# Optimization experiments

Hardware: AMD Instinct MI355X
Metric: run time of the kernel (lower is better)

## Reference

```python
import jax, jax.numpy as jnp
import numpy as np

NEG_SLOPE = 0.2
MASK_FILL = -9e10


def setup_inputs() -> dict:
    key = jax.random.key(0)
    ks = jax.random.split(key, 9)
    B, n_ope, n_mac = 32, 2048, 1024
    total = 64
    ope_dim, mac_dim, out_dim = 64, 64, 128
    ope_ma_adj = jax.random.randint(ks[0], (total, n_ope, n_mac), 0, 2, dtype=jnp.int32)
    batch_idxes = jax.random.randint(ks[1], (B,), 0, total, dtype=jnp.int64)
    feat_ope = jax.random.normal(ks[2], (B, n_ope, ope_dim), dtype=jnp.float32)
    feat_mac = jax.random.normal(ks[3], (B, n_mac, mac_dim), dtype=jnp.float32)
    # parameters (xavier-normal-like scaling)
    def xavier(k, shape):
        fan_in, fan_out = shape[1], shape[0]
        std = jnp.sqrt(2.0 / (fan_in + fan_out))
        return std * jax.random.normal(k, shape, dtype=jnp.float32)
    ope_w = xavier(ks[4], (out_dim, ope_dim))   # Linear weight [out, in]
    mac_w = xavier(ks[5], (out_dim, mac_dim))
    ope_alpha = xavier(ks[6], (out_dim, 1))
    mac_alpha = xavier(ks[7], (out_dim, 1))
    res_w = xavier(ks[8], (out_dim, mac_dim))
    return {
        "ope_ma_adj": ope_ma_adj, "batch_idxes": batch_idxes,
        "feat_ope": feat_ope, "feat_mac": feat_mac,
        "ope_w": ope_w, "mac_w": mac_w,
        "ope_alpha": ope_alpha, "mac_alpha": mac_alpha, "res_w": res_w,
    }


def reference(ope_ma_adj, batch_idxes, feat_ope, feat_mac,
              ope_w, mac_w, ope_alpha, mac_alpha, res_w):
    # dropout p=0 -> identity
    h_ope = jnp.einsum('bod,kd->bok', feat_ope, ope_w)   # [B, n_ope, out]
    h_mac = jnp.einsum('bmd,kd->bmk', feat_mac, mac_w)   # [B, n_mac, out]
    attn_ope = jnp.einsum('bok,k->bo', h_ope, ope_alpha[:, 0])  # [B, n_ope]
    attn_mac = jnp.einsum('bmk,k->bm', h_mac, mac_alpha[:, 0])  # [B, n_mac]
    e = attn_ope[:, :, None] + attn_mac[:, None, :]             # [B, n_ope, n_mac]
    e = jnp.where(e >= 0, e, NEG_SLOPE * e)                      # leaky relu
    mask = ope_ma_adj[batch_idxes] == 1                          # [B, n_ope, n_mac]
    e = jnp.where(mask, e, MASK_FILL)
    alpha = jax.nn.softmax(e, axis=-2)                           # over operations
    out = jnp.einsum('bom,bok->bmk', alpha, h_ope)               # [B, n_mac, out]
    h_res = jnp.einsum('bmd,kd->bmk', feat_mac, res_w)
    return out + h_res
```

## Files before the change

### kernel.cpp

```cpp
#include <hip/hip_runtime.h>

#define N_OPE 2048
#define N_MAC 1024
#define DIM   64
#define KOUT  128
#define NB    32

typedef __attribute__((ext_vector_type(8))) short short8;
typedef __attribute__((ext_vector_type(4))) float floatx4;

static __device__ __forceinline__ unsigned short f2bf(float f) {
    unsigned int u = __builtin_bit_cast(unsigned int, f);
    u += 0x7fffu + ((u >> 16) & 1u);
    return (unsigned short)(u >> 16);
}
static __device__ __forceinline__ float bf2f(unsigned short h) {
    unsigned int u = ((unsigned int)h) << 16;
    return __builtin_bit_cast(float, u);
}

__global__ __launch_bounds__(256, 2) void k_ope(const float* __restrict__ feat,
        const float* __restrict__ w, const float* __restrict__ alpha,
        unsigned short* __restrict__ h_f, float2* __restrict__ pq)
{
    int wid = threadIdx.x >> 6, lane = threadIdx.x & 63;
    int L = lane & 15, q = lane >> 4;
    int base = blockIdx.x * 128 + wid * 32;
    int b = base >> 11;
    int o0w = base & (N_OPE - 1);

    float fA[2][2][8];
    #pragma unroll
    for (int mf = 0; mf < 2; ++mf) {
        const float* fr = feat + (size_t)(base + mf * 16 + L) * DIM + q * 8;
        #pragma unroll
        for (int ks = 0; ks < 2; ++ks) {
            float4 v0 = *(const float4*)(fr + ks * 32);
            float4 v1 = *(const float4*)(fr + ks * 32 + 4);
            fA[mf][ks][0] = v0.x; fA[mf][ks][1] = v0.y; fA[mf][ks][2] = v0.z; fA[mf][ks][3] = v0.w;
            fA[mf][ks][4] = v1.x; fA[mf][ks][5] = v1.y; fA[mf][ks][6] = v1.z; fA[mf][ks][7] = v1.w;
        }
    }

    short8 Ah[2][2], Al[2][2];
    #pragma unroll
    for (int mf = 0; mf < 2; ++mf)
        #pragma unroll
        for (int ks = 0; ks < 2; ++ks)
            #pragma unroll
            for (int j = 0; j < 8; ++j) {
                float x = fA[mf][ks][j];
                unsigned short h = f2bf(x);
                Ah[mf][ks][j] = (short)h;
                Al[mf][ks][j] = (short)f2bf(x - bf2f(h));
            }

    floatx4 C[2][8];
    #pragma unroll
    for (int mf = 0; mf < 2; ++mf)
        #pragma unroll
        for (int nf = 0; nf < 8; ++nf) C[mf][nf] = (floatx4)0.f;

    #pragma unroll
    for (int ks = 0; ks < 2; ++ks) {
        #pragma unroll
        for (int nf = 0; nf < 8; ++nf) {
            const float* wp = w + (size_t)(nf * 16 + L) * DIM + ks * 32 + q * 8;
            float4 u0 = *(const float4*)(wp);
            float4 u1 = *(const float4*)(wp + 4);
            float bw[8] = {u0.x, u0.y, u0.z, u0.w, u1.x, u1.y, u1.z, u1.w};
            short8 Bh, Bl;
            #pragma unroll
            for (int j = 0; j < 8; ++j) {
                unsigned short h = f2bf(bw[j]);
                Bh[j] = (short)h;
                Bl[j] = (short)f2bf(bw[j] - bf2f(h));
            }
            #pragma unroll
            for (int mf = 0; mf < 2; ++mf) {
                C[mf][nf] = __builtin_amdgcn_mfma_f32_16x16x32_bf16(Ah[mf][ks], Bh, C[mf][nf], 0, 0, 0);
                C[mf][nf] = __builtin_amdgcn_mfma_f32_16x16x32_bf16(Al[mf][ks], Bh, C[mf][nf], 0, 0, 0);
                C[mf][nf] = __builtin_amdgcn_mfma_f32_16x16x32_bf16(Ah[mf][ks], Bl, C[mf][nf], 0, 0, 0);
            }
        }
    }

    float alf[8];
    #pragma unroll
    for (int nf = 0; nf < 8; ++nf) alf[nf] = alpha[nf * 16 + L];
    #pragma unroll
    for (int mf = 0; mf < 2; ++mf) {
        #pragma unroll
        for (int r = 0; r < 4; ++r) {
            float s = 0.f;
            #pragma unroll
            for (int nf = 0; nf < 8; ++nf) s = fmaf(C[mf][nf][r], alf[nf], s);
            s += __shfl_xor(s, 1); s += __shfl_xor(s, 2);
            s += __shfl_xor(s, 4); s += __shfl_xor(s, 8);
            if (L == 0)
                pq[base + mf * 16 + q * 4 + r] = make_float2(__expf(s), __expf(0.2f * s));
        }
    }

    __shared__ unsigned short T[4][128 * 40];
    #pragma unroll
    for (int mf = 0; mf < 2; ++mf)
        #pragma unroll
        for (int nf = 0; nf < 8; ++nf)
            #pragma unroll
            for (int r = 0; r < 4; ++r)
                T[wid][(nf * 16 + L) * 40 + mf * 16 + q * 4 + r] = f2bf(C[mf][nf][r]);
    __syncthreads();

    int oc = o0w >> 5;
    unsigned short* dst = h_f + ((((size_t)b * 64 + oc) * 8) * 64 + lane) * 8;
    #pragma unroll
    for (int nf = 0; nf < 8; ++nf) {
        short8 v = *(const short8*)&T[wid][(nf * 16 + L) * 40 + q * 8];
        *(short8*)(dst + (size_t)nf * 512) = v;
    }
}

__global__ __launch_bounds__(256) void k_attn(const int* __restrict__ adj,
        const int* __restrict__ bidx,
        const unsigned short* __restrict__ h_f,
        const float2* __restrict__ pq,
        const float* __restrict__ feat_mac,
        const float* __restrict__ mac_w, const float* __restrict__ mac_alpha,
        const float* __restrict__ res_w,
        float* __restrict__ out)
{
    int b  = blockIdx.y;
    int m0 = blockIdx.x * 32;
    int t = threadIdx.x, wv = t >> 6, lane = t & 63;
    int L = lane & 15, q = lane >> 4;

    __shared__ float buf0[32 * 132];
    __shared__ float buf1[32 * 132];
    __shared__ float waS[64];
    __shared__ float amS[32];
    __shared__ float DS[4][32];

    {
        int d = t & 63, seg = t >> 6;
        float p = 0.f;
        #pragma unroll 8
        for (int n = seg * 32; n < seg * 32 + 32; ++n)
            p = fmaf(mac_w[n * DIM + d], mac_alpha[n], p);
        buf0[seg * 64 + d] = p;
    }
    __syncthreads();
    if (t < 64) waS[t] = buf0[t] + buf0[64 + t] + buf0[128 + t] + buf0[192 + t];
    __syncthreads();
    {
        int row = t & 31, seg = t >> 5;
        const float* fr = feat_mac + ((size_t)b * N_MAC + m0 + row) * DIM + seg * 8;
        float p = 0.f;
        #pragma unroll
        for (int k = 0; k < 8; ++k) p = fmaf(fr[k], waS[seg * 8 + k], p);
        buf1[seg * 32 + row] = p;
    }
    __syncthreads();
    if (t < 32) {
        float s = 0.f;
        #pragma unroll
        for (int sg = 0; sg < 8; ++sg) s += buf1[sg * 32 + t];
        amS[t] = s;
    }
    __syncthreads();

    float2 amv = *(const float2*)&amS[2 * L];
    float pM0 = __expf(amv.x), qM0 = __expf(0.2f * amv.x);
    float pM1 = __expf(amv.y), qM1 = __expf(0.2f * amv.y);

    const int* adjt = adj + (size_t)bidx[b] * (N_OPE * N_MAC);
    const unsigned short* hfb = h_f + (size_t)b * (64 * 8 * 64 * 8);
    const float2* pqb = pq + (size_t)b * N_OPE;

    floatx4 C0[8], C1[8];
    #pragma unroll
    for (int i = 0; i < 8; ++i) { C0[i] = (floatx4)0.f; C1[i] = (floatx4)0.f; }
    float den0 = 0.f, den1 = 0.f;

    int oBeg = wv * (N_OPE / 4);
    for (int o0 = oBeg; o0 < oBeg + N_OPE / 4; o0 += 32) {
        int ob = o0 + q * 8;
        float4 pv0 = *(const float4*)(pqb + ob);
        float4 pv1 = *(const float4*)(pqb + ob + 2);
        float4 pv2 = *(const float4*)(pqb + ob + 4);
        float4 pv3 = *(const float4*)(pqb + ob + 6);
        float pA[8] = {pv0.x, pv0.z, pv1.x, pv1.z, pv2.x, pv2.z, pv3.x, pv3.z};
        float qA[8] = {pv0.y, pv0.w, pv1.y, pv1.w, pv2.y, pv2.w, pv3.y, pv3.w};

        int2 mk[8];
        #pragma unroll
        for (int j = 0; j < 8; ++j)
            mk[j] = *(const int2*)(adjt + (size_t)(ob + j) * N_MAC + m0 + 2 * L);

        const unsigned short* fp = hfb + (((size_t)(o0 >> 5) * 8) * 64 + lane) * 8;
        short8 Bf[8];
        #pragma unroll
        for (int nf = 0; nf < 8; ++nf)
            Bf[nf] = *(const short8*)(fp + (size_t)nf * 512);

        float w0v[8], w1v[8];
        #pragma unroll
        for (int j = 0; j < 8; ++j) {
            float tp0 = pA[j] * pM0;
            float w0 = (tp0 >= 1.0f) ? tp0 : qA[j] * qM0;
            w0 = (mk[j].x == 1) ? w0 : 0.f;
            den0 += w0; w0v[j] = w0;
            float tp1 = pA[j] * pM1;
            float w1 = (tp1 >= 1.0f) ? tp1 : qA[j] * qM1;
            w1 = (mk[j].y == 1) ? w1 : 0.f;
            den1 += w1; w1v[j] = w1;
        }
        int4 A0i, A1i;
        #pragma unroll
        for (int j2 = 0; j2 < 4; ++j2) {
            unsigned lo0 = __builtin_bit_cast(unsigned, w0v[2 * j2])     + 0x8000u;
            unsigned hi0 = __builtin_bit_cast(unsigned, w0v[2 * j2 + 1]) + 0x8000u;
            ((unsigned*)&A0i)[j2] = __builtin_amdgcn_perm(hi0, lo0, 0x07060302u);
            unsigned lo1 = __builtin_bit_cast(unsigned, w1v[2 * j2])     + 0x8000u;
            unsigned hi1 = __builtin_bit_cast(unsigned, w1v[2 * j2 + 1]) + 0x8000u;
            ((unsigned*)&A1i)[j2] = __builtin_amdgcn_perm(hi1, lo1, 0x07060302u);
        }
        short8 A0 = __builtin_bit_cast(short8, A0i);
        short8 A1 = __builtin_bit_cast(short8, A1i);

        #pragma unroll
        for (int nf = 0; nf < 8; ++nf) {
            C0[nf] = __builtin_amdgcn_mfma_f32_16x16x32_bf16(A0, Bf[nf], C0[nf], 0, 0, 0);
            C1[nf] = __builtin_amdgcn_mfma_f32_16x16x32_bf16(A1, Bf[nf], C1[nf], 0, 0, 0);
        }
    }

    den0 += __shfl_xor(den0, 16); den0 += __shfl_xor(den0, 32);
    den1 += __shfl_xor(den1, 16); den1 += __shfl_xor(den1, 32);
    if (q == 0) { DS[wv][L] = den0; DS[wv][16 + L] = den1; }

    if (wv == 0 || wv == 2) {
        float* bp = (wv == 0) ? buf0 : buf1;
        #pragma unroll
        for (int mf = 0; mf < 2; ++mf) {
            const floatx4* Cf = mf ? C1 : C0;
            #pragma unroll
            for (int nf = 0; nf < 8; ++nf)
                #pragma unroll
                for (int r = 0; r < 4; ++r)
                    bp[(mf * 16 + q * 4 + r) * 132 + nf * 16 + L] = Cf[nf][r];
        }
    }
    __syncthreads();
    if (wv == 1 || wv == 3) {
        float* bp = (wv == 1) ? buf0 : buf1;
        #pragma unroll
        for (int mf = 0; mf < 2; ++mf) {
            const floatx4* Cf = mf ? C1 : C0;
            #pragma unroll
            for (int nf = 0; nf < 8; ++nf)
                #pragma unroll
                for (int r = 0; r < 4; ++r)
                    bp[(mf * 16 + q * 4 + r) * 132 + nf * 16 + L] += Cf[nf][r];
        }
    }
    __syncthreads();

    float fA[2][2][8];
    #pragma unroll
    for (int mf = 0; mf < 2; ++mf) {
        const float* fr = feat_mac + ((size_t)b * N_MAC + m0 + 2 * L + mf) * DIM + q * 8;
        #pragma unroll
        for (int ks = 0; ks < 2; ++ks) {
            float4 v0 = *(const float4*)(fr + ks * 32);
            float4 v1 = *(const float4*)(fr + ks * 32 + 4);
            fA[mf][ks][0] = v0.x; fA[mf][ks][1] = v0.y; fA[mf][ks][2] = v0.z; fA[mf][ks][3] = v0.w;
            fA[mf][ks][4] = v1.x; fA[mf][ks][5] = v1.y; fA[mf][ks][6] = v1.z; fA[mf][ks][7] = v1.w;
        }
    }
    short8 Ah[2][2], Al[2][2];
    #pragma unroll
    for (int mf = 0; mf < 2; ++mf)
        #pragma unroll
        for (int ks = 0; ks < 2; ++ks)
            #pragma unroll
            for (int j = 0; j < 8; ++j) {
                float x = fA[mf][ks][j];
                unsigned short h = f2bf(x);
                Ah[mf][ks][j] = (short)h;
                Al[mf][ks][j] = (short)f2bf(x - bf2f(h));
            }
    floatx4 R[2][2];
    R[0][0] = (floatx4)0.f; R[0][1] = (floatx4)0.f;
    R[1][0] = (floatx4)0.f; R[1][1] = (floatx4)0.f;
    #pragma unroll
    for (int ks = 0; ks < 2; ++ks) {
        #pragma unroll
        for (int nfl = 0; nfl < 2; ++nfl) {
            const float* wp = res_w + (size_t)((wv * 2 + nfl) * 16 + L) * DIM + ks * 32 + q * 8;
            float4 u0 = *(const float4*)(wp);
            float4 u1 = *(const float4*)(wp + 4);
            float bw[8] = {u0.x, u0.y, u0.z, u0.w, u1.x, u1.y, u1.z, u1.w};
            short8 Bh, Bl;
            #pragma unroll
            for (int j = 0; j < 8; ++j) {
                unsigned short h = f2bf(bw[j]);
                Bh[j] = (short)h;
                Bl[j] = (short)f2bf(bw[j] - bf2f(h));
            }
            #pragma unroll
            for (int mf = 0; mf < 2; ++mf) {
                R[mf][nfl] = __builtin_amdgcn_mfma_f32_16x16x32_bf16(Ah[mf][ks], Bh, R[mf][nfl], 0, 0, 0);
                R[mf][nfl] = __builtin_amdgcn_mfma_f32_16x16x32_bf16(Al[mf][ks], Bh, R[mf][nfl], 0, 0, 0);
                R[mf][nfl] = __builtin_amdgcn_mfma_f32_16x16x32_bf16(Ah[mf][ks], Bl, R[mf][nfl], 0, 0, 0);
            }
        }
    }

    #pragma unroll
    for (int mf = 0; mf < 2; ++mf) {
        #pragma unroll
        for (int r = 0; r < 4; ++r) {
            int fragrow = q * 4 + r;
            int m = m0 + 2 * fragrow + mf;
            float inv = 1.0f / (DS[0][mf * 16 + fragrow] + DS[1][mf * 16 + fragrow]
                              + DS[2][mf * 16 + fragrow] + DS[3][mf * 16 + fragrow]);
            size_t obase = ((size_t)b * N_MAC + m) * KOUT;
            #pragma unroll
            for (int nfl = 0; nfl < 2; ++nfl) {
                int col = (wv * 2 + nfl) * 16 + L;
                float num = buf0[(mf * 16 + fragrow) * 132 + col]
                          + buf1[(mf * 16 + fragrow) * 132 + col];
                out[obase + col] = num * inv + R[mf][nfl][r];
            }
        }
    }
}

extern "C" void kernel_launch(void* const* d_in, const int* in_sizes, int n_in,
                              void* d_out, int out_size, void* d_ws, size_t ws_size,
                              hipStream_t stream) {
    const int*   adj       = (const int*)d_in[0];
    const int*   bidx      = (const int*)d_in[1];
    const float* feat_ope  = (const float*)d_in[2];
    const float* feat_mac  = (const float*)d_in[3];
    const float* ope_w     = (const float*)d_in[4];
    const float* mac_w     = (const float*)d_in[5];
    const float* ope_alpha = (const float*)d_in[6];
    const float* mac_alpha = (const float*)d_in[7];
    const float* res_w     = (const float*)d_in[8];
    float* out = (float*)d_out;

    char* ws = (char*)d_ws;
    unsigned short* h_f = (unsigned short*)ws;
    float2* pq          = (float2*)(ws + (size_t)(16 << 20));

    k_ope<<<512, 256, 0, stream>>>(feat_ope, ope_w, ope_alpha, h_f, pq);
    k_attn<<<dim3(N_MAC / 32, NB), 256, 0, stream>>>(adj, bidx, h_f, pq, feat_mac,
                                                     mac_w, mac_alpha, res_w, out);
}
```

Measured before the change: 692.0 us.

## Bit-pack adjacency mask in prep kernel and read packed bits in attention

Adds extra blocks to the projection kernel that read each gathered int32 adjacency row once and pack it into 64-bit bitmasks in workspace. The attention kernel then reads one 64-bit word per operation row instead of int2 pairs from the full int32 adjacency. Before, each of the 32 mac-column blocks per batch read its own strided slice of the int32 rows. The change is meant to replace those scattered narrow loads with a single coalesced full-row pass, at the cost of a packed-mask write and read in between and a larger prep launch.

```diff
diff --git a/kernel.cpp b/kernel.cpp
--- a/kernel.cpp
+++ b/kernel.cpp
@@ -19,11 +19,47 @@
     return __builtin_bit_cast(float, u);
 }
 
-__global__ __launch_bounds__(256, 2) void k_ope(const float* __restrict__ feat,
+__global__ __launch_bounds__(256, 2) void k_prep(const float* __restrict__ feat,
         const float* __restrict__ w, const float* __restrict__ alpha,
-        unsigned short* __restrict__ h_f, float2* __restrict__ pq)
+        unsigned short* __restrict__ h_f, float2* __restrict__ pq,
+        const int* __restrict__ adj, const int* __restrict__ bidx,
+        unsigned long long* __restrict__ pk)
 {
     int wid = threadIdx.x >> 6, lane = threadIdx.x & 63;
+
+    if (blockIdx.x >= 512) {
+        int wave = (blockIdx.x - 512) * 4 + wid;
+        int r0 = wave * 32;
+        int b = r0 >> 11;
+        int o0 = r0 & (N_OPE - 1);
+        const int* at = adj + (size_t)bidx[b] * ((size_t)N_OPE * N_MAC);
+        unsigned long long* dst = pk + ((size_t)b * N_OPE + o0) * 16;
+        int L4 = (lane & 15) * 4;
+        #pragma unroll 2
+        for (int i = 0; i < 32; ++i) {
+            const int* rp = at + (size_t)(o0 + i) * N_MAC + lane * 16;
+            int4 a0 = *(const int4*)(rp);
+            int4 a1 = *(const int4*)(rp + 4);
+            int4 a2 = *(const int4*)(rp + 8);
+            int4 a3 = *(const int4*)(rp + 12);
+            unsigned h = (a0.x & 1)        | ((a0.y & 1) << 1)  | ((a0.z & 1) << 2)  | ((a0.w & 1) << 3)
+                       | ((a1.x & 1) << 4) | ((a1.y & 1) << 5)  | ((a1.z & 1) << 6)  | ((a1.w & 1) << 7)
+                       | ((a2.x & 1) << 8) | ((a2.y & 1) << 9)  | ((a2.z & 1) << 10) | ((a2.w & 1) << 11)
+                       | ((a3.x & 1) << 12)| ((a3.y & 1) << 13) | ((a3.z & 1) << 14) | ((a3.w & 1) << 15);
+            unsigned h0 = (unsigned)__shfl((int)h, L4);
+            unsigned h1 = (unsigned)__shfl((int)h, L4 + 1);
+            unsigned h2 = (unsigned)__shfl((int)h, L4 + 2);
+            unsigned h3 = (unsigned)__shfl((int)h, L4 + 3);
+            unsigned long long W = (unsigned long long)(h0 & 0xffffu)
+                                 | ((unsigned long long)(h1 & 0xffffu) << 16)
+                                 | ((unsigned long long)(h2 & 0xffffu) << 32)
+                                 | ((unsigned long long)(h3 & 0xffffu) << 48);
+            if (lane < 16)
+                dst[(size_t)i * 16 + lane] = W;
+        }
+        return;
+    }
+
     int L = lane & 15, q = lane >> 4;
     int base = blockIdx.x * 128 + wid * 32;
     int b = base >> 11;
@@ -121,8 +157,8 @@
     }
 }
 
-__global__ __launch_bounds__(256) void k_attn(const int* __restrict__ adj,
-        const int* __restrict__ bidx,
+__global__ __launch_bounds__(256) void k_attn(
+        const unsigned long long* __restrict__ pk,
         const unsigned short* __restrict__ h_f,
         const float2* __restrict__ pq,
         const float* __restrict__ feat_mac,
@@ -173,9 +209,11 @@
     float pM0 = __expf(amv.x), qM0 = __expf(0.2f * amv.x);
     float pM1 = __expf(amv.y), qM1 = __expf(0.2f * amv.y);
 
-    const int* adjt = adj + (size_t)bidx[b] * (N_OPE * N_MAC);
+    const unsigned long long* pkb = pk + (size_t)b * N_OPE * 16;
     const unsigned short* hfb = h_f + (size_t)b * (64 * 8 * 64 * 8);
     const float2* pqb = pq + (size_t)b * N_OPE;
+    int wi = m0 >> 6;
+    int sft = (m0 & 63) + 2 * L;
 
     floatx4 C0[8], C1[8];
     #pragma unroll
@@ -192,10 +230,10 @@
         float pA[8] = {pv0.x, pv0.z, pv1.x, pv1.z, pv2.x, pv2.z, pv3.x, pv3.z};
         float qA[8] = {pv0.y, pv0.w, pv1.y, pv1.w, pv2.y, pv2.w, pv3.y, pv3.w};
 
-        int2 mk[8];
+        unsigned long long wm[8];
         #pragma unroll
         for (int j = 0; j < 8; ++j)
-            mk[j] = *(const int2*)(adjt + (size_t)(ob + j) * N_MAC + m0 + 2 * L);
+            wm[j] = pkb[(size_t)(ob + j) * 16 + wi];
 
         const unsigned short* fp = hfb + (((size_t)(o0 >> 5) * 8) * 64 + lane) * 8;
         short8 Bf[8];
@@ -208,11 +246,11 @@
         for (int j = 0; j < 8; ++j) {
             float tp0 = pA[j] * pM0;
             float w0 = (tp0 >= 1.0f) ? tp0 : qA[j] * qM0;
-            w0 = (mk[j].x == 1) ? w0 : 0.f;
+            w0 = ((wm[j] >> sft) & 1ull) ? w0 : 0.f;
             den0 += w0; w0v[j] = w0;
             float tp1 = pA[j] * pM1;
             float w1 = (tp1 >= 1.0f) ? tp1 : qA[j] * qM1;
-            w1 = (mk[j].y == 1) ? w1 : 0.f;
+            w1 = ((wm[j] >> (sft + 1)) & 1ull) ? w1 : 0.f;
             den1 += w1; w1v[j] = w1;
         }
         int4 A0i, A1i;
@@ -354,8 +392,9 @@
     char* ws = (char*)d_ws;
     unsigned short* h_f = (unsigned short*)ws;
     float2* pq          = (float2*)(ws + (size_t)(16 << 20));
-
-    k_ope<<<512, 256, 0, stream>>>(feat_ope, ope_w, ope_alpha, h_f, pq);
-    k_attn<<<dim3(N_MAC / 32, NB), 256, 0, stream>>>(adj, bidx, h_f, pq, feat_mac,
+    unsigned long long* pk = (unsigned long long*)(ws + (size_t)(17 << 20));
+
+    k_prep<<<1024, 256, 0, stream>>>(feat_ope, ope_w, ope_alpha, h_f, pq, adj, bidx, pk);
+    k_attn<<<dim3(N_MAC / 32, NB), 256, 0, stream>>>(pk, h_f, pq, feat_mac,
                                                      mac_w, mac_alpha, res_w, out);
 }
```

Result: slower. 708.9 us (+2.4%).
